# Kernel tuning notes

Measured on AMD Instinct MI355X. Metric: run time of the kernel, lower is better.

The kernel has to match this reference:

```python
import math
import jax, jax.numpy as jnp
import numpy as np

D_MODEL = 1024
NUM_HEADS = 16
HEAD_DIM = D_MODEL // NUM_HEADS
THETA = 10000.0
MAX_SEQ_LEN = 2048
BATCH = 4
SEQ = 2048


def _rope_tables():
    # angles[i, j] = i / theta**(2j/d_k), shapes [max_seq_len, head_dim//2]
    i = jnp.arange(MAX_SEQ_LEN, dtype=jnp.float32)
    k = jnp.arange(0, HEAD_DIM, 2, dtype=jnp.float32) / HEAD_DIM
    angles = i[:, None] * (1.0 / (THETA ** k))[None, :]
    return jnp.cos(angles), jnp.sin(angles)


def _apply_rope(x, token_positions, cos_tab, sin_tab):
    # x: [b, h, s, d_k]; token_positions: [s]
    b, h, s, dk = x.shape
    xr = x.reshape(b, h, s, dk // 2, 2)
    x0, x1 = xr[..., 0], xr[..., 1]
    cos_pos = cos_tab[token_positions]  # [s, dk//2]
    sin_pos = sin_tab[token_positions]
    x0_rot = x0 * cos_pos - x1 * sin_pos
    x1_rot = x0 * sin_pos + x1 * cos_pos
    return jnp.stack([x0_rot, x1_rot], axis=-1).reshape(x.shape)


def setup_inputs() -> dict:
    key = jax.random.key(0)
    k1, k2, k3 = jax.random.split(key, 3)
    std_qkv = math.sqrt(2.0 / (D_MODEL + 3 * D_MODEL))
    std_o = math.sqrt(2.0 / (D_MODEL + D_MODEL))
    return {
        "x": jax.random.normal(k1, (BATCH, SEQ, D_MODEL), dtype=jnp.float32),
        "token_positions": jnp.arange(SEQ, dtype=jnp.int64) if jax.config.jax_enable_x64 else jnp.arange(SEQ, dtype=jnp.int32),
        "qkv_w": jax.random.normal(k2, (3 * D_MODEL, D_MODEL), dtype=jnp.float32) * std_qkv,
        "o_w": jax.random.normal(k3, (D_MODEL, D_MODEL), dtype=jnp.float32) * std_o,
    }


def reference(x, token_positions, qkv_w, o_w):
    b, s, _ = x.shape
    cos_tab, sin_tab = _rope_tables()
    # fused QKV projection: [b, s, 3*d_model]
    qkv = jnp.einsum('bsd,ed->bse', x, qkv_w)
    qkv = qkv.reshape(b, s, 3, NUM_HEADS, HEAD_DIM)
    q = jnp.transpose(qkv[:, :, 0], (0, 2, 1, 3))  # [b, h, s, hd]
    k = jnp.transpose(qkv[:, :, 1], (0, 2, 1, 3))
    v = jnp.transpose(qkv[:, :, 2], (0, 2, 1, 3))
    q = _apply_rope(q, token_positions, cos_tab, sin_tab)
    k = _apply_rope(k, token_positions, cos_tab, sin_tab)
    # causal mask and eager softmax attention (full [b,h,s,s] scores)
    scores = jnp.einsum('bhnk,bhmk->bhnm', q, k) / math.sqrt(HEAD_DIM)
    causal = jnp.tril(jnp.ones((s, s), dtype=bool))
    scores = jnp.where(causal, scores, -jnp.inf)
    attn = jax.nn.softmax(scores, axis=-1)
    ctx = jnp.einsum('bhnm,bhmv->bhnv', attn, v)
    ctx = jnp.transpose(ctx, (0, 2, 1, 3)).reshape(b, s, D_MODEL)
    return jnp.einsum('bsd,ed->bse', ctx, o_w)
```

## Files before the change

kernel.cpp:

```cpp
#include <hip/hip_runtime.h>


#define DM   1024
#define NH   16
#define HD   64
#define SEQL 2048
#define BATCH 4
#define QKV_ELEMS 8388608

using short8 = __attribute__((ext_vector_type(8))) short;
using f32x4  = __attribute__((ext_vector_type(4))) float;
typedef unsigned short u16;

#define WAIT_VM(n) __builtin_amdgcn_s_waitcnt(0x0F70 | (n))
#define BARRIER()  __builtin_amdgcn_s_barrier()

__device__ __forceinline__ u16 f2bf(float f) {
    unsigned u = __builtin_bit_cast(unsigned, f);
    u += 0x7fffu + ((u >> 16) & 1u);
    return (u16)(u >> 16);
}
__device__ __forceinline__ float bf2f(u16 h) {
    unsigned u = ((unsigned)h) << 16;
    return __builtin_bit_cast(float, u);
}
__device__ __forceinline__ unsigned pk2bf(float a, float b) {
    return (unsigned)f2bf(a) | ((unsigned)f2bf(b) << 16);
}
__device__ __forceinline__ float fexp2(float x) {
#if __has_builtin(__builtin_amdgcn_exp2f)
    return __builtin_amdgcn_exp2f(x);
#else
    return __expf(x * 0.6931471805599453f);
#endif
}

__device__ __forceinline__ void load16(const void* g, void* l) {
    __builtin_amdgcn_global_load_lds(
        (__attribute__((address_space(1))) unsigned int*)(unsigned long long)g,
        (__attribute__((address_space(3))) unsigned int*)(unsigned int)(unsigned long long)l,
        16, 0, 0);
}

__global__ __launch_bounds__(256) void prep(const float* __restrict__ x, u16* __restrict__ xb,
                                            const float* __restrict__ qw, u16* __restrict__ wb,
                                            const float* __restrict__ ow, u16* __restrict__ owb,
                                            float* __restrict__ cost, float* __restrict__ sint) {
    int bx = blockIdx.x;
    if (bx < 12288) {
        const float* in; u16* out; int i;
        if (bx < 8192)       { in = x;  out = xb;  i = bx * 256 + threadIdx.x; }
        else if (bx < 11264) { in = qw; out = wb;  i = (bx - 8192) * 256 + threadIdx.x; }
        else                 { in = ow; out = owb; i = (bx - 11264) * 256 + threadIdx.x; }
        float4 v = ((const float4*)in)[i];
        uint2 o;
        o.x = pk2bf(v.x, v.y);
        o.y = pk2bf(v.z, v.w);
        ((uint2*)out)[i] = o;
    } else {
        int t = (bx - 12288) * 256 + threadIdx.x;
        int j = t & 31, pos = t >> 5;
        float freq = exp2f((float)j * (-2.0f / 64.0f) * 13.287712379549449f);
        float ang = (float)pos * freq;
        cost[t] = cosf(ang);
        sint[t] = sinf(ang);
    }
}

__device__ __forceinline__ void gemm128_core(const u16* __restrict__ A,
                                             const u16* __restrict__ B,
                                             int K, int m0, int n0,
                                             u16* As, u16* Bs, f32x4 acc[4][4]) {
    int tid = threadIdx.x, w = tid >> 6, l = tid & 63;
    int l15 = l & 15, l4 = l >> 4;
    int wm = w >> 1, wn = w & 1;
    int r0 = 32 * w + (l >> 2);
    int gblk = ((l & 3) ^ ((l >> 4) & 3)) * 8;
    const u16* gA0 = A + (size_t)(m0 + r0) * K + gblk;
    const u16* gA1 = gA0 + (size_t)16 * K;
    const u16* gB0 = B + (size_t)(n0 + r0) * K + gblk;
    const u16* gB1 = gB0 + (size_t)16 * K;
    char* ldsA = (char*)As + 2048 * w;
    char* ldsB = (char*)Bs + 2048 * w;
    int fo = ((l4 ^ (l15 >> 2)) & 3) * 16;
    f32x4 z = {0.f, 0.f, 0.f, 0.f};
#pragma unroll
    for (int i = 0; i < 4; ++i)
#pragma unroll
        for (int j = 0; j < 4; ++j) acc[i][j] = z;
    int nk = K >> 5;
#pragma unroll
    for (int t = 0; t < 2; ++t) {
        int ko = t << 5, nb = t * 8192;
        load16(gA0 + ko, ldsA + nb); load16(gA1 + ko, ldsA + nb + 1024);
        load16(gB0 + ko, ldsB + nb); load16(gB1 + ko, ldsB + nb + 1024);
    }
    int buf = 0;
    for (int kt = 0; kt < nk; ++kt) {
        if (kt < nk - 1) WAIT_VM(4); else WAIT_VM(0);
        BARRIER();
        if (kt + 2 < nk) {
            int ko = (kt + 2) << 5;
            int nb = 8192 * ((buf + 2) % 3);
            load16(gA0 + ko, ldsA + nb); load16(gA1 + ko, ldsA + nb + 1024);
            load16(gB0 + ko, ldsB + nb); load16(gB1 + ko, ldsB + nb + 1024);
        }
        const char* bA = (const char*)As + 8192 * buf;
        const char* bB = (const char*)Bs + 8192 * buf;
        short8 a[4], b[4];
#pragma unroll
        for (int i = 0; i < 4; ++i)
            a[i] = *(const short8*)(bA + (64 * wm + 16 * i + l15) * 64 + fo);
#pragma unroll
        for (int j = 0; j < 4; ++j)
            b[j] = *(const short8*)(bB + (64 * wn + 16 * j + l15) * 64 + fo);
#pragma unroll
        for (int i = 0; i < 4; ++i)
#pragma unroll
            for (int j = 0; j < 4; ++j)
                acc[i][j] = __builtin_amdgcn_mfma_f32_16x16x32_bf16(a[i], b[j], acc[i][j], 0, 0, 0);
        buf = (buf + 1) % 3;
    }
}

__global__ __launch_bounds__(256) void gemm_qkv(const u16* __restrict__ xb,
                                                const u16* __restrict__ wb,
                                                u16* __restrict__ qkv,
                                                u16* __restrict__ vt,
                                                const int* __restrict__ pos_ids,
                                                const float* __restrict__ cost,
                                                const float* __restrict__ sint) {
    __shared__ __align__(16) u16 As[3 * 128 * 32], Bs[3 * 128 * 32];
    f32x4 acc[4][4];
    int m0 = blockIdx.y * 128, n0 = blockIdx.x * 128;
    gemm128_core(xb, wb, DM, m0, n0, As, Bs, acc);
    int l = threadIdx.x & 63, w = threadIdx.x >> 6;
    int l15 = l & 15, l4 = l >> 4;
    int wm = w >> 1, wn = w & 1;
    if (blockIdx.x >= 16) {
#pragma unroll
        for (int j = 0; j < 4; ++j) {
            int nV = (n0 - 2048) + 64 * wn + 16 * j + l15;
            int h = nV >> 6, d = nV & 63;
#pragma unroll
            for (int i = 0; i < 4; ++i) {
                int sb = m0 + 64 * wm + 16 * i + 4 * l4;
                int b = sb >> 11, s = sb & 2047;
                uint2 pk;
                pk.x = pk2bf(acc[i][j][0], acc[i][j][1]);
                pk.y = pk2bf(acc[i][j][2], acc[i][j][3]);
                *(uint2*)&vt[((size_t)(b * 16 + h) * HD + d) * SEQL + s] = pk;
            }
        }
    } else {
        float sc = (blockIdx.x < 8) ? 0.18033688011112042f : 1.0f;
#pragma unroll
        for (int j = 0; j < 4; ++j) {
            int n = n0 + 64 * wn + 16 * j + l15;
            int which = n >> 10, h = (n >> 6) & 15, d = n & 63;
            int d2 = d >> 1;
            u16* base = qkv + (size_t)which * QKV_ELEMS;
#pragma unroll
            for (int i = 0; i < 4; ++i) {
#pragma unroll
                for (int r = 0; r < 4; ++r) {
                    int m = m0 + 64 * wm + 16 * i + 4 * l4 + r;
                    int b = m >> 11, s = m & 2047;
                    int pos = pos_ids[s];
                    float c  = cost[pos * 32 + d2];
                    float sn = sint[pos * 32 + d2];
                    float v  = acc[i][j][r];
                    float vp = __shfl_xor(v, 1);
                    float o  = (d & 1) ? (vp * sn + v * c) : (v * c - vp * sn);
                    base[((size_t)(b * 16 + h) * SEQL + s) * HD + d] = f2bf(o * sc);
                }
            }
        }
    }
}

__global__ __launch_bounds__(256) void gemm_out(const u16* __restrict__ ctx,
                                                const u16* __restrict__ owb,
                                                float* __restrict__ out) {
    __shared__ __align__(16) u16 As[3 * 128 * 32], Bs[3 * 128 * 32];
    f32x4 acc[4][4];
    int m0 = blockIdx.y * 128, n0 = blockIdx.x * 128;
    gemm128_core(ctx, owb, DM, m0, n0, As, Bs, acc);
    int l = threadIdx.x & 63, w = threadIdx.x >> 6;
    int l15 = l & 15, l4 = l >> 4;
    int wm = w >> 1, wn = w & 1;
#pragma unroll
    for (int i = 0; i < 4; ++i) {
        int mb = m0 + 64 * wm + 16 * i + 4 * l4;
#pragma unroll
        for (int j = 0; j < 4; ++j) {
            int n = n0 + 64 * wn + 16 * j + l15;
#pragma unroll
            for (int r = 0; r < 4; ++r)
                out[(size_t)(mb + r) * DM + n] = acc[i][j][r];
        }
    }
}

__device__ __forceinline__ void flash_pass(int qt, const u16* __restrict__ Qb,
                                           const u16* __restrict__ Kb,
                                           const u16* __restrict__ Vb,
                                           u16* __restrict__ ctx, int bh,
                                           u16* KsB, u16* VsB, u16* PsB) {
    int tid = threadIdx.x, w = tid >> 6, l = tid & 63;
    int l15 = l & 15, l4 = l >> 4;
    int q0 = qt * 256;
    int swz = l15 & 7;
    int b0 = (l4 ^ swz) * 16;

    short8 aq[2][2];
#pragma unroll
    for (int g = 0; g < 2; ++g) {
        const u16* qr = Qb + (size_t)(q0 + 128 * g + 16 * w + l15) * HD;
        aq[g][0] = *(const short8*)&qr[l4 * 8];
        aq[g][1] = *(const short8*)&qr[32 + l4 * 8];
    }
    int srow = l >> 3;
    int sblk = ((l & 7) ^ srow) * 8;
    const u16* gK = Kb + (size_t)(8 * w + srow) * HD + sblk;
    const u16* gV = Vb + (size_t)(8 * w + srow) * SEQL + sblk;
    char* ldsK = (char*)KsB + 1024 * w;
    char* ldsV = (char*)VsB + 1024 * w;
    char* prow = (char*)PsB + 2048 * w + l15 * 128;

    f32x4 z = {0.f, 0.f, 0.f, 0.f};
    f32x4 O[2][4] = {{z, z, z, z}, {z, z, z, z}};
    float lsum[2] = {0.f, 0.f};
    int nk = 4 * qt + 4;
    int d0 = 4 * qt + (w >> 2);
    int rowlim = 16 * (w & 3) + l15;

    BARRIER();
#pragma unroll
    for (int t = 0; t < 2; ++t) {
        load16(gK + (size_t)(t * 64) * HD, ldsK + t * 8192);
        load16(gV + t * 64,                ldsV + t * 8192);
    }
    int buf = 0;
    for (int it = 0; it < nk; ++it) {
        if (it < nk - 1) WAIT_VM(2); else WAIT_VM(0);
        BARRIER();
        if (it + 2 < nk) {
            int k0n = (it + 2) * 64;
            int nb = 8192 * ((buf + 2) % 3);
            load16(gK + (size_t)k0n * HD, ldsK + nb);
            load16(gV + k0n,              ldsV + nb);
        }
        if (it <= d0 + 2) {
            const char* bK = (const char*)KsB + 8192 * buf;
            const char* bV = (const char*)VsB + 8192 * buf;
            short8 kf[4][2], vf[4][2];
#pragma unroll
            for (int c = 0; c < 4; ++c) {
                const char* kr = bK + (16 * c + l15) * 128;
                kf[c][0] = *(const short8*)(kr + b0);
                kf[c][1] = *(const short8*)(kr + (b0 ^ 64));
                const char* vr = bV + (16 * c + l15) * 128;
                vf[c][0] = *(const short8*)(vr + b0);
                vf[c][1] = *(const short8*)(vr + (b0 ^ 64));
            }
#pragma unroll
            for (int g = 0; g < 2; ++g) {
                int dg = d0 + 2 * g;
                if (it > dg) continue;
                f32x4 S[4];
#pragma unroll
                for (int c = 0; c < 4; ++c) {
                    S[c] = __builtin_amdgcn_mfma_f32_16x16x32_bf16(kf[c][0], aq[g][0], z, 0, 0, 0);
                    S[c] = __builtin_amdgcn_mfma_f32_16x16x32_bf16(kf[c][1], aq[g][1], S[c], 0, 0, 0);
                }
                if (it == dg) {
#pragma unroll
                    for (int c = 0; c < 4; ++c)
#pragma unroll
                        for (int r = 0; r < 4; ++r)
                            if (16 * c + 4 * l4 + r > rowlim) S[c][r] = -3e38f;
                }
#pragma unroll
                for (int c = 0; c < 4; ++c)
#pragma unroll
                    for (int r = 0; r < 4; ++r) {
                        float p = fexp2(S[c][r]);
                        S[c][r] = p;
                        lsum[g] += p;
                    }
#pragma unroll
                for (int c = 0; c < 4; ++c) {
                    uint2 pk;
                    pk.x = pk2bf(S[c][0], S[c][1]);
                    pk.y = pk2bf(S[c][2], S[c][3]);
                    *(uint2*)(prow + ((((2 * c + (l4 >> 1)) ^ swz) << 4) | ((l4 & 1) << 3))) = pk;
                }
                short8 ap0 = *(const short8*)(prow + b0);
                short8 ap1 = *(const short8*)(prow + (b0 ^ 64));
#pragma unroll
                for (int nt = 0; nt < 4; ++nt) {
                    O[g][nt] = __builtin_amdgcn_mfma_f32_16x16x32_bf16(ap0, vf[nt][0], O[g][nt], 0, 0, 0);
                    O[g][nt] = __builtin_amdgcn_mfma_f32_16x16x32_bf16(ap1, vf[nt][1], O[g][nt], 0, 0, 0);
                }
            }
        }
        buf = (buf + 1) % 3;
    }
    int b = bh >> 4, h = bh & 15;
#pragma unroll
    for (int g = 0; g < 2; ++g) {
        float ls = lsum[g];
        ls += __shfl_xor(ls, 16);
        ls += __shfl_xor(ls, 32);
        float linv[4];
#pragma unroll
        for (int r = 0; r < 4; ++r) linv[r] = 1.0f / __shfl(ls, 20 * l4 + r);
#pragma unroll
        for (int nt = 0; nt < 4; ++nt) {
            int d = 16 * nt + l15;
#pragma unroll
            for (int r = 0; r < 4; ++r) {
                int s = q0 + 128 * g + 16 * w + 4 * l4 + r;
                ctx[((size_t)(b * SEQL + s)) * DM + h * 64 + d] = f2bf(O[g][nt][r] * linv[r]);
            }
        }
    }
}

__global__ __launch_bounds__(512, 2) void flash_attn(const u16* __restrict__ Q,
                                                     const u16* __restrict__ K,
                                                     const u16* __restrict__ Vt,
                                                     u16* __restrict__ ctx) {
    __shared__ __align__(16) u16 Ks[3][64 * 64];
    __shared__ __align__(16) u16 Vs[3][64 * 64];
    __shared__ __align__(16) u16 Ps[8][16 * 64];
    int bh = blockIdx.y, pair = blockIdx.x;
    const u16* Qb = Q + (size_t)bh * SEQL * HD;
    const u16* Kb = K + (size_t)bh * SEQL * HD;
    const u16* Vb = Vt + (size_t)bh * HD * SEQL;
    flash_pass(7 - pair, Qb, Kb, Vb, ctx, bh, &Ks[0][0], &Vs[0][0], &Ps[0][0]);
    flash_pass(pair,     Qb, Kb, Vb, ctx, bh, &Ks[0][0], &Vs[0][0], &Ps[0][0]);
}

extern "C" void kernel_launch(void* const* d_in, const int* in_sizes, int n_in,
                              void* d_out, int out_size, void* d_ws, size_t ws_size,
                              hipStream_t stream) {
    const float* x     = (const float*)d_in[0];
    const int*   pos   = (const int*)d_in[1];
    const float* qkv_w = (const float*)d_in[2];
    const float* o_w   = (const float*)d_in[3];
    float* out = (float*)d_out;

    char* ws = (char*)d_ws;
    u16*   xb   = (u16*)(ws);
    u16*   wb   = (u16*)(ws + 16777216);
    u16*   owb  = (u16*)(ws + 23068672);
    float* cost = (float*)(ws + 25165824);
    float* sint = (float*)(ws + 25427968);
    u16*   qkv  = (u16*)(ws + 25690112);
    u16*   vt   = (u16*)(ws + 76021760);
    u16*   ctx  = xb;

    prep<<<12544, 256, 0, stream>>>(x, xb, qkv_w, wb, o_w, owb, cost, sint);
    gemm_qkv<<<dim3(24, 64), 256, 0, stream>>>(xb, wb, qkv, vt, pos, cost, sint);
    flash_attn<<<dim3(4, 64), 512, 0, stream>>>(qkv, qkv + QKV_ELEMS, vt, ctx);
    gemm_out<<<dim3(8, 64), 256, 0, stream>>>(ctx, owb, out);
}
```

Baseline: 246.1 us.

## Enlarge QKV GEMM tile to 256x256 with 8 waves and swizzled block order

Replaces the 128x128 QKV projection GEMM with a 256x256 tile computed by 512 threads (8 waves, each 128x64). It adds an XOR-swizzled LDS layout, an interleaved schedule that splits the A and B global loads around two MFMA phases with setprio, and a block-index swizzle for L2 locality. The larger tile raises arithmetic intensity and cuts global reloads of the input and weight operands. In exchange it doubles LDS use, raises register pressure from 32 accumulators per thread, and leaves only 384 blocks, which may limit occupancy and tail balance.

```diff
diff --git a/kernel.cpp b/kernel.cpp
--- a/kernel.cpp
+++ b/kernel.cpp
@@ -13,6 +13,7 @@
 typedef unsigned short u16;
 
 #define WAIT_VM(n) __builtin_amdgcn_s_waitcnt(0x0F70 | (n))
+#define WAIT_LGKM0() __builtin_amdgcn_s_waitcnt(0xC07F)
 #define BARRIER()  __builtin_amdgcn_s_barrier()
 
 __device__ __forceinline__ u16 f2bf(float f) {
@@ -123,56 +124,134 @@
     }
 }
 
-__global__ __launch_bounds__(256) void gemm_qkv(const u16* __restrict__ xb,
-                                                const u16* __restrict__ wb,
-                                                u16* __restrict__ qkv,
-                                                u16* __restrict__ vt,
-                                                const int* __restrict__ pos_ids,
-                                                const float* __restrict__ cost,
-                                                const float* __restrict__ sint) {
-    __shared__ __align__(16) u16 As[3 * 128 * 32], Bs[3 * 128 * 32];
-    f32x4 acc[4][4];
-    int m0 = blockIdx.y * 128, n0 = blockIdx.x * 128;
-    gemm128_core(xb, wb, DM, m0, n0, As, Bs, acc);
-    int l = threadIdx.x & 63, w = threadIdx.x >> 6;
+__global__ __launch_bounds__(512, 2) void gemm_qkv(const u16* __restrict__ xb,
+                                                   const u16* __restrict__ wb,
+                                                   u16* __restrict__ qkv,
+                                                   u16* __restrict__ vt,
+                                                   const int* __restrict__ pos_ids,
+                                                   const float* __restrict__ cost,
+                                                   const float* __restrict__ sint) {
+    __shared__ __align__(16) u16 As[3 * 256 * 32];
+    __shared__ __align__(16) u16 Bs[3 * 256 * 32];
+    int tid = threadIdx.x, w = tid >> 6, l = tid & 63;
     int l15 = l & 15, l4 = l >> 4;
-    int wm = w >> 1, wn = w & 1;
-    if (blockIdx.x >= 16) {
+    int wr = w >> 2, wc = w & 3;
+
+    int bid = blockIdx.y * 12 + blockIdx.x;
+    int swz = (bid & 7) * 48 + (bid >> 3);
+    int nI = swz % 12, mI = swz / 12;
+    int m0 = mI * 256, n0 = nI * 256;
+
+    int schunk = ((l & 3) ^ ((l >> 3) & 3)) * 8;
+    const u16* gA = xb + (size_t)(m0 + 32 * w + (l >> 2)) * DM + schunk;
+    const u16* gB = wb + (size_t)(n0 + 32 * w + (l >> 2)) * DM + schunk;
+    char* ldsA = (char*)As + 2048 * w;
+    char* ldsB = (char*)Bs + 2048 * w;
+
+    int roff = (l4 ^ ((l15 >> 1) & 3)) * 16;
+    int aoff = (128 * wr + l15) * 64 + roff;
+    int boff = (64 * wc + l15) * 64 + roff;
+
+    f32x4 acc[8][4];
+    f32x4 z = {0.f, 0.f, 0.f, 0.f};
+#pragma unroll
+    for (int i = 0; i < 8; ++i)
+#pragma unroll
+        for (int j = 0; j < 4; ++j) acc[i][j] = z;
+
+#pragma unroll
+    for (int t = 0; t < 2; ++t) {
+        load16(gA + t * 32,           ldsA + t * 16384);
+        load16(gA + t * 32 + 16 * DM, ldsA + t * 16384 + 1024);
+        load16(gB + t * 32,           ldsB + t * 16384);
+        load16(gB + t * 32 + 16 * DM, ldsB + t * 16384 + 1024);
+    }
+    WAIT_VM(4);
+    BARRIER();
+
+    int buf = 0;
+    for (int kt = 0; kt < 32; ++kt) {
+        const char* bA = (const char*)As + 16384 * buf;
+        const char* bB = (const char*)Bs + 16384 * buf;
+        int nb = buf + 2; if (nb >= 3) nb -= 3;
+        short8 a[4], b[4];
+#pragma unroll
+        for (int i = 0; i < 4; ++i) a[i] = *(const short8*)(bA + aoff + 1024 * i);
+#pragma unroll
+        for (int j = 0; j < 4; ++j) b[j] = *(const short8*)(bB + boff + 1024 * j);
+        if (kt + 2 < 32) {
+            load16(gA + (kt + 2) * 32,           ldsA + nb * 16384);
+            load16(gA + (kt + 2) * 32 + 16 * DM, ldsA + nb * 16384 + 1024);
+        }
+        BARRIER();
+        WAIT_LGKM0();
+        __builtin_amdgcn_s_setprio(1);
+#pragma unroll
+        for (int i = 0; i < 4; ++i)
+#pragma unroll
+            for (int j = 0; j < 4; ++j)
+                acc[i][j] = __builtin_amdgcn_mfma_f32_16x16x32_bf16(a[i], b[j], acc[i][j], 0, 0, 0);
+        __builtin_amdgcn_s_setprio(0);
+        BARRIER();
+        short8 a2[4];
+#pragma unroll
+        for (int i = 0; i < 4; ++i) a2[i] = *(const short8*)(bA + aoff + 1024 * (i + 4));
+        if (kt + 2 < 32) {
+            load16(gB + (kt + 2) * 32,           ldsB + nb * 16384);
+            load16(gB + (kt + 2) * 32 + 16 * DM, ldsB + nb * 16384 + 1024);
+        }
+        BARRIER();
+        WAIT_LGKM0();
+        __builtin_amdgcn_s_setprio(1);
+#pragma unroll
+        for (int i = 0; i < 4; ++i)
+#pragma unroll
+            for (int j = 0; j < 4; ++j)
+                acc[i + 4][j] = __builtin_amdgcn_mfma_f32_16x16x32_bf16(a2[i], b[j], acc[i + 4][j], 0, 0, 0);
+        __builtin_amdgcn_s_setprio(0);
+        if (kt + 2 < 32) WAIT_VM(4); else WAIT_VM(0);
+        BARRIER();
+        buf = buf + 1; if (buf >= 3) buf = 0;
+    }
+
+    if (nI >= 8) {
 #pragma unroll
         for (int j = 0; j < 4; ++j) {
-            int nV = (n0 - 2048) + 64 * wn + 16 * j + l15;
-            int h = nV >> 6, d = nV & 63;
-#pragma unroll
-            for (int i = 0; i < 4; ++i) {
-                int sb = m0 + 64 * wm + 16 * i + 4 * l4;
-                int b = sb >> 11, s = sb & 2047;
+            int nv = (n0 - 2048) + 64 * wc + 16 * j + l15;
+            int h = nv >> 6, d = nv & 63;
+#pragma unroll
+            for (int i = 0; i < 8; ++i) {
+                int sb = m0 + 128 * wr + 16 * i + 4 * l4;
+                int bb = sb >> 11, s = sb & 2047;
                 uint2 pk;
                 pk.x = pk2bf(acc[i][j][0], acc[i][j][1]);
                 pk.y = pk2bf(acc[i][j][2], acc[i][j][3]);
-                *(uint2*)&vt[((size_t)(b * 16 + h) * HD + d) * SEQL + s] = pk;
+                *(uint2*)&vt[((size_t)(bb * 16 + h) * HD + d) * SEQL + s] = pk;
             }
         }
     } else {
-        float sc = (blockIdx.x < 8) ? 0.18033688011112042f : 1.0f;
-#pragma unroll
-        for (int j = 0; j < 4; ++j) {
-            int n = n0 + 64 * wn + 16 * j + l15;
-            int which = n >> 10, h = (n >> 6) & 15, d = n & 63;
-            int d2 = d >> 1;
-            u16* base = qkv + (size_t)which * QKV_ELEMS;
-#pragma unroll
-            for (int i = 0; i < 4; ++i) {
-#pragma unroll
-                for (int r = 0; r < 4; ++r) {
-                    int m = m0 + 64 * wm + 16 * i + 4 * l4 + r;
-                    int b = m >> 11, s = m & 2047;
-                    int pos = pos_ids[s];
-                    float c  = cost[pos * 32 + d2];
-                    float sn = sint[pos * 32 + d2];
+        float sc = (nI < 4) ? 0.18033688011112042f : 1.0f;
+        u16* base = qkv + (size_t)(nI >> 2) * QKV_ELEMS;
+        int h = ((n0 & 1023) >> 6) + wc;
+#pragma unroll
+        for (int i = 0; i < 8; ++i) {
+#pragma unroll
+            for (int r = 0; r < 4; ++r) {
+                int m = m0 + 128 * wr + 16 * i + 4 * l4 + r;
+                int bb = m >> 11, s = m & 2047;
+                int pos = pos_ids[s];
+                const float* cr = cost + pos * 32;
+                const float* sr = sint + pos * 32;
+                u16* orow = base + ((size_t)(bb * 16 + h) * SEQL + s) * HD;
+#pragma unroll
+                for (int j = 0; j < 4; ++j) {
+                    int d = 16 * j + l15, d2 = d >> 1;
+                    float c  = cr[d2];
+                    float sn = sr[d2];
                     float v  = acc[i][j][r];
                     float vp = __shfl_xor(v, 1);
                     float o  = (d & 1) ? (vp * sn + v * c) : (v * c - vp * sn);
-                    base[((size_t)(b * 16 + h) * SEQL + s) * HD + d] = f2bf(o * sc);
+                    orow[d] = f2bf(o * sc);
                 }
             }
         }
@@ -363,7 +442,7 @@
     u16*   ctx  = xb;
 
     prep<<<12544, 256, 0, stream>>>(x, xb, qkv_w, wb, o_w, owb, cost, sint);
-    gemm_qkv<<<dim3(24, 64), 256, 0, stream>>>(xb, wb, qkv, vt, pos, cost, sint);
+    gemm_qkv<<<dim3(12, 32), 512, 0, stream>>>(xb, wb, qkv, vt, pos, cost, sint);
     flash_attn<<<dim3(4, 64), 512, 0, stream>>>(qkv, qkv + QKV_ELEMS, vt, ctx);
     gemm_out<<<dim3(8, 64), 256, 0, stream>>>(ctx, owb, out);
 }
```

After: 247.4 us. About the same (+0.5%).
